# Optimization experiments

Hardware: AMD Instinct MI355X
Metric: run time of the kernel (lower is better)

Reference implementation:

```python
import jax, jax.numpy as jnp
import numpy as np

N_HEADS = 16


def setup_inputs() -> dict:
    key = jax.random.key(0)
    k1, k2 = jax.random.split(key)
    bs, width, length = 8, 3 * N_HEADS * 64, 1024  # C=64 per head
    qkv = jax.random.normal(k1, (bs, width, length), dtype=jnp.float32)
    mask = jax.random.uniform(k2, (bs, length), dtype=jnp.float32)
    return {"qkv": qkv, "mask": mask}


def reference(qkv, mask):
    bs, width, length = qkv.shape
    ch = width // (3 * N_HEADS)
    q, k, v = jnp.split(qkv, 3, axis=1)
    # view(bs*H, ch, T): head index is inner (b*H + h ordering)
    q = q.reshape(bs * N_HEADS, ch, length)
    k = k.reshape(bs * N_HEADS, ch, length)
    v = v.reshape(bs * N_HEADS, ch, length)
    scale = 1.0 / jnp.sqrt(jnp.sqrt(jnp.asarray(ch, dtype=qkv.dtype)))
    # [bs*H, T, T] score matrix
    weight = jnp.einsum('bct,bcs->bts', q * scale, k * scale)
    # torch mask.repeat(n_heads, 1) tiles the batch dim -> jnp.tile
    m = jnp.tile(mask, (N_HEADS, 1))[:, None, :]  # [bs*H, 1, T]
    weight = weight * m
    weight = jax.nn.softmax(weight.astype(jnp.float32), axis=-1).astype(weight.dtype)
    a = jnp.einsum('bts,bcs->bct', weight, v)  # [bs*H, ch, T]
    return a.reshape(bs, N_HEADS * ch, length)
```

## Files before the change

kernel.cpp:

```cpp
#include <hip/hip_runtime.h>
#include <stdint.h>
#include <math.h>

typedef float  f32x4  __attribute__((ext_vector_type(4)));
typedef __bf16 bf16x8 __attribute__((ext_vector_type(8)));
typedef __bf16 bf16x4 __attribute__((ext_vector_type(4)));

#define MFMA16(a, b, c) __builtin_amdgcn_mfma_f32_16x16x32_bf16((a), (b), (c), 0, 0, 0)
#define EXP2(x) __builtin_amdgcn_exp2f(x)

static constexpr int kT = 1024;

static constexpr int kTileEl = 4096;
static constexpr size_t kTensorEl    = (size_t)128 * 16 * kTileEl;
static constexpr size_t kTensorBytes = kTensorEl * 2;

static constexpr int kLS = 72;

__device__ inline void async16(const void* g, void* l) {
  __builtin_amdgcn_global_load_lds(
      (const __attribute__((address_space(1))) void*)g,
      (__attribute__((address_space(3))) void*)l, 16, 0, 0);
}

__global__ __launch_bounds__(256, 4)
void prepass(const float* __restrict__ qkv, const float* __restrict__ mask,
             __bf16* __restrict__ kh, __bf16* __restrict__ vh)
{
  __shared__ float tsK[64 * 65];
  __shared__ float tsV[64 * 65];
  const int tid = threadIdx.x;
  const int bid = blockIdx.x, bh = bid >> 4, tile = bid & 15;
  const int b = bh >> 4, h = bh & 15, t0 = tile * 64;
  const float* __restrict__ kb = qkv + (size_t)(b * 3072 + 1024 + h * 64) * kT;
  const float* __restrict__ vb = qkv + (size_t)(b * 3072 + 2048 + h * 64) * kT;
  const float* __restrict__ mrow = mask + (size_t)(h & 7) * kT;
  const size_t tbase = ((size_t)bh * 16 + tile) * kTileEl;

  const int t4   = (tid & 15) * 4;
  const int crow = tid >> 4;
  const f32x4 m4 = *(const f32x4*)&mrow[t0 + t4];
  #pragma unroll
  for (int i = 0; i < 4; ++i) {
    const int c = i * 16 + crow;
    f32x4 k4 = *(const f32x4*)&kb[(size_t)c * kT + t0 + t4];
    f32x4 v4 = *(const f32x4*)&vb[(size_t)c * kT + t0 + t4];
    k4 *= m4;
    *(f32x4*)&tsK[c * 65 + t4] = k4;
    *(f32x4*)&tsV[c * 65 + t4] = v4;
  }
  __syncthreads();

  #pragma unroll
  for (int i = 0; i < 2; ++i) {
    const int p = i * 256 + tid;
    const int chunk = p >> 6, pl = p & 63;
    const int rr  = (chunk >> 1) * 16 + (pl & 15);
    const int kc0 = (chunk & 1) * 32 + (pl >> 4) * 8;
    bf16x8 k8, v8;
    #pragma unroll
    for (int j = 0; j < 8; ++j) {
      k8[j] = (__bf16)tsK[(kc0 + j) * 65 + rr];
      v8[j] = (__bf16)tsV[rr * 65 + kc0 + j];
    }
    *(bf16x8*)&kh[tbase + (size_t)p * 8] = k8;
    *(bf16x8*)&vh[tbase + (size_t)p * 8] = v8;
  }
}

__global__ __launch_bounds__(256, 3)
void attn_main(const float* __restrict__ qkv,
               const __bf16* __restrict__ kh, const __bf16* __restrict__ vh,
               float* __restrict__ out)
{
  __shared__ __align__(16) char smem[49152];

  const int tid  = threadIdx.x;
  const int lane = tid & 63;
  const int wave = tid >> 6;
  const int quad = lane >> 4;
  const int l15  = lane & 15;

  const int bid = blockIdx.x;
  const int bh  = bid & 127;
  const int tp  = bid >> 7;
  const int b   = bh >> 4;
  const int h   = bh & 15;
  const int t0  = tp * 128;
  const size_t hbase = (size_t)bh * 16;

  {
    const char* g = (const char*)(kh + hbase * kTileEl) + (size_t)lane * 16;
    for (int i = wave; i < 16; i += 4) async16(g + i * 1024, smem + i * 1024);
  }

  bf16x8 qh[2][2], ql[2][2];
  {
    float* ts = (float*)(smem + 32512);
    const float* __restrict__ qb = qkv + (size_t)(b * 3072 + h * 64) * kT;
    const int t4   = (tid & 15) * 4;
    const int crow = tid >> 4;
    const int trow = wave * 16 + l15;
    #pragma unroll
    for (int half = 0; half < 2; ++half) {
      const int tq0 = t0 + half * 64;
      #pragma unroll
      for (int i = 0; i < 4; ++i) {
        const int c = i * 16 + crow;
        f32x4 q4 = *(const f32x4*)&qb[(size_t)c * kT + tq0 + t4];
        q4 *= 0.18033688f;
        *(f32x4*)&ts[c * 65 + t4] = q4;
      }
      __syncthreads();
      #pragma unroll
      for (int kc = 0; kc < 2; ++kc) {
        bf16x8 hf, lf;
        #pragma unroll
        for (int j = 0; j < 8; ++j) {
          float q = ts[(kc * 32 + quad * 8 + j) * 65 + trow];
          __bf16 hi = (__bf16)q;
          hf[j] = hi;
          lf[j] = (__bf16)(q - (float)hi);
        }
        qh[half][kc] = hf;
        ql[half][kc] = lf;
      }
      __syncthreads();
    }
  }

  f32x4 O0[4], O1[4];
  #pragma unroll
  for (int cc = 0; cc < 4; ++cc) {
    O0[cc] = (f32x4){0.f, 0.f, 0.f, 0.f};
    O1[cc] = (f32x4){0.f, 0.f, 0.f, 0.f};
  }
  f32x4 la0 = (f32x4){0.f, 0.f, 0.f, 0.f};
  f32x4 la1 = (f32x4){0.f, 0.f, 0.f, 0.f};

  char* sP0 = smem + 32768 + wave * 4096;
  char* sP1 = sP0 + 2048;
  const int pwr = (l15 << 4) + ((quad & 1) << 3) + ((quad >> 1) << 8);

  for (int p = 0; p < 8; ++p) {
    __syncthreads();

    const __bf16* __restrict__ vt0 = vh + (hbase + 2 * p) * kTileEl;
    const __bf16* __restrict__ vt1 = vt0 + kTileEl;

    bf16x8 vA0[4], vA1[4];
    #pragma unroll
    for (int cc = 0; cc < 4; ++cc)
      vA0[cc] = *(const bf16x8*)&vt0[(size_t)(cc * 2) * 512 + lane * 8];
    #pragma unroll
    for (int cc = 0; cc < 4; ++cc)
      vA1[cc] = *(const bf16x8*)&vt0[(size_t)(cc * 2 + 1) * 512 + lane * 8];

    if (p < 7) {
      const char* g = (const char*)(kh + (hbase + 2 * (p + 1)) * kTileEl) + (size_t)lane * 16;
      char* l = smem + ((p + 1) & 1) * 16384;
      for (int i = wave; i < 16; i += 4) async16(g + i * 1024, l + i * 1024);
    }

    {
      const __bf16* __restrict__ sKt = (const __bf16*)(smem + (p & 1) * 16384);

      #pragma unroll
      for (int sc = 0; sc < 4; ++sc) {
        bf16x8 k0 = *(const bf16x8*)&sKt[(size_t)(sc * 2) * 512 + lane * 8];
        bf16x8 k1 = *(const bf16x8*)&sKt[(size_t)(sc * 2 + 1) * 512 + lane * 8];
        f32x4 a0 = (f32x4){0.f, 0.f, 0.f, 0.f};
        f32x4 a1 = (f32x4){0.f, 0.f, 0.f, 0.f};
        a0 = MFMA16(k0, ql[0][0], a0);
        a1 = MFMA16(k0, ql[1][0], a1);
        a0 = MFMA16(k0, qh[0][0], a0);
        a1 = MFMA16(k0, qh[1][0], a1);
        a0 = MFMA16(k1, ql[0][1], a0);
        a1 = MFMA16(k1, ql[1][1], a1);
        a0 = MFMA16(k1, qh[0][1], a0);
        a1 = MFMA16(k1, qh[1][1], a1);
        f32x4 e0, e1;
        #pragma unroll
        for (int r = 0; r < 4; ++r) {
          e0[r] = EXP2(a0[r]);
          e1[r] = EXP2(a1[r]);
        }
        la0 += e0;
        la1 += e1;
        bf16x4 p0, p1;
        #pragma unroll
        for (int r = 0; r < 4; ++r) {
          p0[r] = (__bf16)e0[r];
          p1[r] = (__bf16)e1[r];
        }
        const int po = ((sc >> 1) << 10) + ((sc & 1) << 9) + pwr;
        *(bf16x4*)(sP0 + po) = p0;
        *(bf16x4*)(sP1 + po) = p1;
      }

      bf16x8 pb00 = *(const bf16x8*)(sP0 + lane * 16);
      bf16x8 pb01 = *(const bf16x8*)(sP0 + 1024 + lane * 16);
      bf16x8 pb10 = *(const bf16x8*)(sP1 + lane * 16);
      bf16x8 pb11 = *(const bf16x8*)(sP1 + 1024 + lane * 16);

      #pragma unroll
      for (int cc = 0; cc < 4; ++cc) {
        O0[cc] = MFMA16(vA0[cc], pb00, O0[cc]);
        O1[cc] = MFMA16(vA0[cc], pb10, O1[cc]);
        O0[cc] = MFMA16(vA1[cc], pb01, O0[cc]);
        O1[cc] = MFMA16(vA1[cc], pb11, O1[cc]);
      }
    }

    {
      const __bf16* __restrict__ sKt = (const __bf16*)(smem + (p & 1) * 16384 + 8192);

      bf16x8 vB0[4], vB1[4];
      #pragma unroll
      for (int cc = 0; cc < 4; ++cc)
        vB0[cc] = *(const bf16x8*)&vt1[(size_t)(cc * 2) * 512 + lane * 8];

      #pragma unroll
      for (int sc = 0; sc < 4; ++sc) {
        bf16x8 k0 = *(const bf16x8*)&sKt[(size_t)(sc * 2) * 512 + lane * 8];
        bf16x8 k1 = *(const bf16x8*)&sKt[(size_t)(sc * 2 + 1) * 512 + lane * 8];
        f32x4 a0 = (f32x4){0.f, 0.f, 0.f, 0.f};
        f32x4 a1 = (f32x4){0.f, 0.f, 0.f, 0.f};
        a0 = MFMA16(k0, ql[0][0], a0);
        a1 = MFMA16(k0, ql[1][0], a1);
        a0 = MFMA16(k0, qh[0][0], a0);
        a1 = MFMA16(k0, qh[1][0], a1);
        a0 = MFMA16(k1, ql[0][1], a0);
        a1 = MFMA16(k1, ql[1][1], a1);
        a0 = MFMA16(k1, qh[0][1], a0);
        a1 = MFMA16(k1, qh[1][1], a1);
        f32x4 e0, e1;
        #pragma unroll
        for (int r = 0; r < 4; ++r) {
          e0[r] = EXP2(a0[r]);
          e1[r] = EXP2(a1[r]);
        }
        la0 += e0;
        la1 += e1;
        bf16x4 p0, p1;
        #pragma unroll
        for (int r = 0; r < 4; ++r) {
          p0[r] = (__bf16)e0[r];
          p1[r] = (__bf16)e1[r];
        }
        const int po = ((sc >> 1) << 10) + ((sc & 1) << 9) + pwr;
        *(bf16x4*)(sP0 + po) = p0;
        *(bf16x4*)(sP1 + po) = p1;
      }

      #pragma unroll
      for (int cc = 0; cc < 4; ++cc)
        vB1[cc] = *(const bf16x8*)&vt1[(size_t)(cc * 2 + 1) * 512 + lane * 8];

      bf16x8 pb00 = *(const bf16x8*)(sP0 + lane * 16);
      bf16x8 pb01 = *(const bf16x8*)(sP0 + 1024 + lane * 16);
      bf16x8 pb10 = *(const bf16x8*)(sP1 + lane * 16);
      bf16x8 pb11 = *(const bf16x8*)(sP1 + 1024 + lane * 16);

      #pragma unroll
      for (int cc = 0; cc < 4; ++cc) {
        O0[cc] = MFMA16(vB0[cc], pb00, O0[cc]);
        O1[cc] = MFMA16(vB0[cc], pb10, O1[cc]);
        O0[cc] = MFMA16(vB1[cc], pb01, O0[cc]);
        O1[cc] = MFMA16(vB1[cc], pb11, O1[cc]);
      }
    }
  }

  float ls0 = la0[0] + la0[1] + la0[2] + la0[3];
  float ls1 = la1[0] + la1[1] + la1[2] + la1[3];
  ls0 += __shfl_xor(ls0, 16);
  ls0 += __shfl_xor(ls0, 32);
  ls1 += __shfl_xor(ls1, 16);
  ls1 += __shfl_xor(ls1, 32);
  const float inv0 = 1.0f / ls0;
  const float inv1 = 1.0f / ls1;

  const int tcol = t0 + wave * 16 + l15;
  float* __restrict__ obase = out + (size_t)b * (1024 * 1024) + (size_t)(h * 64) * kT;
  #pragma unroll
  for (int cc = 0; cc < 4; ++cc) {
    #pragma unroll
    for (int r = 0; r < 4; ++r) {
      const int c = cc * 16 + quad * 4 + r;
      obase[(size_t)c * kT + tcol]      = O0[cc][r] * inv0;
      obase[(size_t)c * kT + tcol + 64] = O1[cc][r] * inv1;
    }
  }
}

__global__ __launch_bounds__(256, 2)
void attn_fused(const float* __restrict__ qkv, const float* __restrict__ mask,
                float* __restrict__ out)
{
  __shared__ __align__(16) __bf16 Ahi[64 * kLS];
  __shared__ __align__(16) __bf16 Alo[64 * kLS];
  __shared__ __align__(16) __bf16 Vhi[64 * kLS];
  __shared__ __align__(16) __bf16 Vlo[64 * kLS];
  __shared__ __align__(16) __bf16 Phi[64 * kLS];
  __shared__ __align__(16) __bf16 Plo[64 * kLS];
  __shared__ __align__(16) float  ms[64];

  const int tid  = threadIdx.x;
  const int lane = tid & 63;
  const int wave = tid >> 6;
  const int quad = lane >> 4;
  const int l15  = lane & 15;

  const int bid = blockIdx.x;
  const int bh  = bid >> 4;
  const int tb  = bid & 15;
  const int b   = bh >> 4;
  const int h   = bh & 15;
  const int t0  = tb * 64;

  const float* __restrict__ qbase = qkv + (size_t)(b * 3072 + h * 64) * kT;
  const float* __restrict__ kbase = qkv + (size_t)(b * 3072 + 1024 + h * 64) * kT;
  const float* __restrict__ vbase = qkv + (size_t)(b * 3072 + 2048 + h * 64) * kT;
  const float* __restrict__ mrow  = mask + (size_t)(h & 7) * kT;

  const int sl = tid & 63;
  const int cg = tid >> 6;

  #pragma unroll
  for (int i = 0; i < 16; ++i) {
    const int c = cg * 16 + i;
    float v  = qbase[(size_t)c * kT + t0 + sl] * 0.125f;
    __bf16 hi = (__bf16)v;
    Ahi[sl * kLS + c] = hi;
    Alo[sl * kLS + c] = (__bf16)(v - (float)hi);
  }
  __syncthreads();

  bf16x8 qh[2], ql[2];
  {
    const int row = (wave * 16 + l15) * kLS;
    #pragma unroll
    for (int kc = 0; kc < 2; ++kc) {
      qh[kc] = *(const bf16x8*)&Ahi[row + kc * 32 + quad * 8];
      ql[kc] = *(const bf16x8*)&Alo[row + kc * 32 + quad * 8];
    }
  }
  __syncthreads();

  f32x4 O[4];
  #pragma unroll
  for (int cc = 0; cc < 4; ++cc) O[cc] = (f32x4){0.f, 0.f, 0.f, 0.f};
  float m_run = -__builtin_inff();
  float l_run = 0.f;

  for (int s0 = 0; s0 < kT; s0 += 64) {
    #pragma unroll
    for (int i = 0; i < 16; ++i) {
      const int c = cg * 16 + i;
      float kv   = kbase[(size_t)c * kT + s0 + sl];
      __bf16 khi = (__bf16)kv;
      Ahi[sl * kLS + c] = khi;
      Alo[sl * kLS + c] = (__bf16)(kv - (float)khi);
      float vv   = vbase[(size_t)c * kT + s0 + sl];
      __bf16 vhi = (__bf16)vv;
      Vhi[c * kLS + sl] = vhi;
      Vlo[c * kLS + sl] = (__bf16)(vv - (float)vhi);
    }
    if (tid < 64) ms[tid] = mrow[s0 + tid];
    __syncthreads();

    f32x4 S[4];
    #pragma unroll
    for (int sc = 0; sc < 4; ++sc) {
      f32x4 acc = (f32x4){0.f, 0.f, 0.f, 0.f};
      #pragma unroll
      for (int kc = 0; kc < 2; ++kc) {
        const int off = (sc * 16 + l15) * kLS + kc * 32 + quad * 8;
        bf16x8 kh8 = *(const bf16x8*)&Ahi[off];
        bf16x8 kl8 = *(const bf16x8*)&Alo[off];
        acc = MFMA16(kh8, ql[kc], acc);
        acc = MFMA16(kl8, qh[kc], acc);
        acc = MFMA16(kh8, qh[kc], acc);
      }
      S[sc] = acc;
    }

    float x[16];
    float tmax = -__builtin_inff();
    #pragma unroll
    for (int sc = 0; sc < 4; ++sc) {
      f32x4 mv = *(const f32x4*)&ms[sc * 16 + quad * 4];
      #pragma unroll
      for (int r = 0; r < 4; ++r) {
        float xv = S[sc][r] * mv[r];
        x[sc * 4 + r] = xv;
        tmax = fmaxf(tmax, xv);
      }
    }
    tmax = fmaxf(tmax, __shfl_xor(tmax, 16));
    tmax = fmaxf(tmax, __shfl_xor(tmax, 32));
    const float mnew  = fmaxf(m_run, tmax);
    const float alpha = __expf(m_run - mnew);
    float tsum = 0.f;
    #pragma unroll
    for (int i = 0; i < 16; ++i) {
      float p = __expf(x[i] - mnew);
      x[i] = p;
      tsum += p;
    }
    tsum += __shfl_xor(tsum, 16);
    tsum += __shfl_xor(tsum, 32);
    l_run = l_run * alpha + tsum;
    m_run = mnew;
    #pragma unroll
    for (int cc = 0; cc < 4; ++cc) O[cc] = O[cc] * alpha;

    const int prow = (wave * 16 + l15) * kLS;
    #pragma unroll
    for (int sc = 0; sc < 4; ++sc) {
      bf16x4 ph, pl;
      #pragma unroll
      for (int r = 0; r < 4; ++r) {
        float p   = x[sc * 4 + r];
        __bf16 hi = (__bf16)p;
        ph[r] = hi;
        pl[r] = (__bf16)(p - (float)hi);
      }
      *(bf16x4*)&Phi[prow + sc * 16 + quad * 4] = ph;
      *(bf16x4*)&Plo[prow + sc * 16 + quad * 4] = pl;
    }
    __syncthreads();

    bf16x8 pbh[2], pbl[2];
    #pragma unroll
    for (int kc = 0; kc < 2; ++kc) {
      pbh[kc] = *(const bf16x8*)&Phi[prow + kc * 32 + quad * 8];
      pbl[kc] = *(const bf16x8*)&Plo[prow + kc * 32 + quad * 8];
    }
    #pragma unroll
    for (int cc = 0; cc < 4; ++cc) {
      #pragma unroll
      for (int kc = 0; kc < 2; ++kc) {
        const int off = (cc * 16 + l15) * kLS + kc * 32 + quad * 8;
        bf16x8 v8 = *(const bf16x8*)&Vhi[off];
        bf16x8 w8 = *(const bf16x8*)&Vlo[off];
        O[cc] = MFMA16(v8, pbl[kc], O[cc]);
        O[cc] = MFMA16(w8, pbh[kc], O[cc]);
        O[cc] = MFMA16(v8, pbh[kc], O[cc]);
      }
    }
    __syncthreads();
  }

  const float inv  = 1.0f / l_run;
  const int   tcol = t0 + wave * 16 + l15;
  float* __restrict__ obase = out + (size_t)b * (1024 * 1024) + (size_t)(h * 64) * kT;
  #pragma unroll
  for (int cc = 0; cc < 4; ++cc) {
    #pragma unroll
    for (int r = 0; r < 4; ++r) {
      const int c = cc * 16 + quad * 4 + r;
      obase[(size_t)c * kT + tcol] = O[cc][r] * inv;
    }
  }
}

extern "C" void kernel_launch(void* const* d_in, const int* in_sizes, int n_in,
                              void* d_out, int out_size, void* d_ws, size_t ws_size,
                              hipStream_t stream)
{
  const float* qkv  = (const float*)d_in[0];
  const float* mask = (const float*)d_in[1];
  float* out = (float*)d_out;
  (void)in_sizes; (void)n_in; (void)out_size;

  if (ws_size >= 2 * kTensorBytes) {
    char* w = (char*)d_ws;
    __bf16* kh = (__bf16*)(w + 0 * kTensorBytes);
    __bf16* vh = (__bf16*)(w + 1 * kTensorBytes);
    prepass<<<dim3(2048), dim3(256), 0, stream>>>(qkv, mask, kh, vh);
    attn_main<<<dim3(1024), dim3(256), 0, stream>>>(qkv, kh, vh, out);
  } else {
    attn_fused<<<dim3(2048), dim3(256), 0, stream>>>(qkv, mask, out);
  }
}
```

Before: 203.9 us.

## Process 256 query rows per block to reuse K/V tiles across four query groups

Each attn_main block now handles 256 query positions instead of 128: it holds four groups of Q fragments and accumulators per wave and launches half as many blocks. Every K tile loaded into LDS and every V fragment read from global memory is reused across four query groups instead of two, which halves K/V traffic per query. In exchange, register pressure and LDS use rise (64KB shared, launch bounds lowered to 2 blocks per CU), and the grid shrinks to 512 blocks. That may underfill the GPU's CUs and lower occupancy.

```diff
diff --git a/kernel.cpp b/kernel.cpp
--- a/kernel.cpp
+++ b/kernel.cpp
@@ -68,12 +68,12 @@
   }
 }
 
-__global__ __launch_bounds__(256, 3)
+__global__ __launch_bounds__(256, 2)
 void attn_main(const float* __restrict__ qkv,
                const __bf16* __restrict__ kh, const __bf16* __restrict__ vh,
                float* __restrict__ out)
 {
-  __shared__ __align__(16) char smem[49152];
+  __shared__ __align__(16) char smem[65536];
 
   const int tid  = threadIdx.x;
   const int lane = tid & 63;
@@ -83,10 +83,10 @@
 
   const int bid = blockIdx.x;
   const int bh  = bid & 127;
-  const int tp  = bid >> 7;
+  const int tq  = bid >> 7;
   const int b   = bh >> 4;
   const int h   = bh & 15;
-  const int t0  = tp * 128;
+  const int t0  = tq * 256;
   const size_t hbase = (size_t)bh * 16;
 
   {
@@ -94,15 +94,15 @@
     for (int i = wave; i < 16; i += 4) async16(g + i * 1024, smem + i * 1024);
   }
 
-  bf16x8 qh[2][2], ql[2][2];
+  bf16x8 qh[4][2], ql[4][2];
   {
-    float* ts = (float*)(smem + 32512);
+    float* ts = (float*)(smem + 32768);
     const float* __restrict__ qb = qkv + (size_t)(b * 3072 + h * 64) * kT;
     const int t4   = (tid & 15) * 4;
     const int crow = tid >> 4;
     const int trow = wave * 16 + l15;
     #pragma unroll
-    for (int half = 0; half < 2; ++half) {
+    for (int half = 0; half < 4; ++half) {
       const int tq0 = t0 + half * 64;
       #pragma unroll
       for (int i = 0; i < 4; ++i) {
@@ -129,17 +129,16 @@
     }
   }
 
-  f32x4 O0[4], O1[4];
-  #pragma unroll
-  for (int cc = 0; cc < 4; ++cc) {
-    O0[cc] = (f32x4){0.f, 0.f, 0.f, 0.f};
-    O1[cc] = (f32x4){0.f, 0.f, 0.f, 0.f};
-  }
-  f32x4 la0 = (f32x4){0.f, 0.f, 0.f, 0.f};
-  f32x4 la1 = (f32x4){0.f, 0.f, 0.f, 0.f};
-
-  char* sP0 = smem + 32768 + wave * 4096;
-  char* sP1 = sP0 + 2048;
+  f32x4 O[4][4];
+  f32x4 la[4];
+  #pragma unroll
+  for (int hh = 0; hh < 4; ++hh) {
+    la[hh] = (f32x4){0.f, 0.f, 0.f, 0.f};
+    #pragma unroll
+    for (int cc = 0; cc < 4; ++cc) O[hh][cc] = (f32x4){0.f, 0.f, 0.f, 0.f};
+  }
+
+  char* sPw = smem + 32768 + wave * 8192;
   const int pwr = (l15 << 4) + ((quad & 1) << 3) + ((quad >> 1) << 8);
 
   for (int p = 0; p < 8; ++p) {
@@ -169,46 +168,40 @@
       for (int sc = 0; sc < 4; ++sc) {
         bf16x8 k0 = *(const bf16x8*)&sKt[(size_t)(sc * 2) * 512 + lane * 8];
         bf16x8 k1 = *(const bf16x8*)&sKt[(size_t)(sc * 2 + 1) * 512 + lane * 8];
-        f32x4 a0 = (f32x4){0.f, 0.f, 0.f, 0.f};
-        f32x4 a1 = (f32x4){0.f, 0.f, 0.f, 0.f};
-        a0 = MFMA16(k0, ql[0][0], a0);
-        a1 = MFMA16(k0, ql[1][0], a1);
-        a0 = MFMA16(k0, qh[0][0], a0);
-        a1 = MFMA16(k0, qh[1][0], a1);
-        a0 = MFMA16(k1, ql[0][1], a0);
-        a1 = MFMA16(k1, ql[1][1], a1);
-        a0 = MFMA16(k1, qh[0][1], a0);
-        a1 = MFMA16(k1, qh[1][1], a1);
-        f32x4 e0, e1;
-        #pragma unroll
-        for (int r = 0; r < 4; ++r) {
-          e0[r] = EXP2(a0[r]);
-          e1[r] = EXP2(a1[r]);
+        f32x4 a[4];
+        #pragma unroll
+        for (int hh = 0; hh < 4; ++hh) a[hh] = (f32x4){0.f, 0.f, 0.f, 0.f};
+        #pragma unroll
+        for (int hh = 0; hh < 4; ++hh) a[hh] = MFMA16(k0, ql[hh][0], a[hh]);
+        #pragma unroll
+        for (int hh = 0; hh < 4; ++hh) a[hh] = MFMA16(k0, qh[hh][0], a[hh]);
+        #pragma unroll
+        for (int hh = 0; hh < 4; ++hh) a[hh] = MFMA16(k1, ql[hh][1], a[hh]);
+        #pragma unroll
+        for (int hh = 0; hh < 4; ++hh) a[hh] = MFMA16(k1, qh[hh][1], a[hh]);
+        const int po = ((sc >> 1) << 10) + ((sc & 1) << 9) + pwr;
+        #pragma unroll
+        for (int hh = 0; hh < 4; ++hh) {
+          f32x4 e;
+          #pragma unroll
+          for (int r = 0; r < 4; ++r) e[r] = EXP2(a[hh][r]);
+          la[hh] += e;
+          bf16x4 pp;
+          #pragma unroll
+          for (int r = 0; r < 4; ++r) pp[r] = (__bf16)e[r];
+          *(bf16x4*)(sPw + hh * 2048 + po) = pp;
         }
-        la0 += e0;
-        la1 += e1;
-        bf16x4 p0, p1;
-        #pragma unroll
-        for (int r = 0; r < 4; ++r) {
-          p0[r] = (__bf16)e0[r];
-          p1[r] = (__bf16)e1[r];
+      }
+
+      #pragma unroll
+      for (int hh = 0; hh < 4; ++hh) {
+        bf16x8 pb0 = *(const bf16x8*)(sPw + hh * 2048 + lane * 16);
+        bf16x8 pb1 = *(const bf16x8*)(sPw + hh * 2048 + 1024 + lane * 16);
+        #pragma unroll
+        for (int cc = 0; cc < 4; ++cc) {
+          O[hh][cc] = MFMA16(vA0[cc], pb0, O[hh][cc]);
+          O[hh][cc] = MFMA16(vA1[cc], pb1, O[hh][cc]);
         }
-        const int po = ((sc >> 1) << 10) + ((sc & 1) << 9) + pwr;
-        *(bf16x4*)(sP0 + po) = p0;
-        *(bf16x4*)(sP1 + po) = p1;
-      }
-
-      bf16x8 pb00 = *(const bf16x8*)(sP0 + lane * 16);
-      bf16x8 pb01 = *(const bf16x8*)(sP0 + 1024 + lane * 16);
-      bf16x8 pb10 = *(const bf16x8*)(sP1 + lane * 16);
-      bf16x8 pb11 = *(const bf16x8*)(sP1 + 1024 + lane * 16);
-
-      #pragma unroll
-      for (int cc = 0; cc < 4; ++cc) {
-        O0[cc] = MFMA16(vA0[cc], pb00, O0[cc]);
-        O1[cc] = MFMA16(vA0[cc], pb10, O1[cc]);
-        O0[cc] = MFMA16(vA1[cc], pb01, O0[cc]);
-        O1[cc] = MFMA16(vA1[cc], pb11, O1[cc]);
       }
     }
 
@@ -224,72 +217,62 @@
       for (int sc = 0; sc < 4; ++sc) {
         bf16x8 k0 = *(const bf16x8*)&sKt[(size_t)(sc * 2) * 512 + lane * 8];
         bf16x8 k1 = *(const bf16x8*)&sKt[(size_t)(sc * 2 + 1) * 512 + lane * 8];
-        f32x4 a0 = (f32x4){0.f, 0.f, 0.f, 0.f};
-        f32x4 a1 = (f32x4){0.f, 0.f, 0.f, 0.f};
-        a0 = MFMA16(k0, ql[0][0], a0);
-        a1 = MFMA16(k0, ql[1][0], a1);
-        a0 = MFMA16(k0, qh[0][0], a0);
-        a1 = MFMA16(k0, qh[1][0], a1);
-        a0 = MFMA16(k1, ql[0][1], a0);
-        a1 = MFMA16(k1, ql[1][1], a1);
-        a0 = MFMA16(k1, qh[0][1], a0);
-        a1 = MFMA16(k1, qh[1][1], a1);
-        f32x4 e0, e1;
-        #pragma unroll
-        for (int r = 0; r < 4; ++r) {
-          e0[r] = EXP2(a0[r]);
-          e1[r] = EXP2(a1[r]);
+        f32x4 a[4];
+        #pragma unroll
+        for (int hh = 0; hh < 4; ++hh) a[hh] = (f32x4){0.f, 0.f, 0.f, 0.f};
+        #pragma unroll
+        for (int hh = 0; hh < 4; ++hh) a[hh] = MFMA16(k0, ql[hh][0], a[hh]);
+        #pragma unroll
+        for (int hh = 0; hh < 4; ++hh) a[hh] = MFMA16(k0, qh[hh][0], a[hh]);
+        #pragma unroll
+        for (int hh = 0; hh < 4; ++hh) a[hh] = MFMA16(k1, ql[hh][1], a[hh]);
+        #pragma unroll
+        for (int hh = 0; hh < 4; ++hh) a[hh] = MFMA16(k1, qh[hh][1], a[hh]);
+        const int po = ((sc >> 1) << 10) + ((sc & 1) << 9) + pwr;
+        #pragma unroll
+        for (int hh = 0; hh < 4; ++hh) {
+          f32x4 e;
+          #pragma unroll
+          for (int r = 0; r < 4; ++r) e[r] = EXP2(a[hh][r]);
+          la[hh] += e;
+          bf16x4 pp;
+          #pragma unroll
+          for (int r = 0; r < 4; ++r) pp[r] = (__bf16)e[r];
+          *(bf16x4*)(sPw + hh * 2048 + po) = pp;
         }
-        la0 += e0;
-        la1 += e1;
-        bf16x4 p0, p1;
-        #pragma unroll
-        for (int r = 0; r < 4; ++r) {
-          p0[r] = (__bf16)e0[r];
-          p1[r] = (__bf16)e1[r];
-        }
-        const int po = ((sc >> 1) << 10) + ((sc & 1) << 9) + pwr;
-        *(bf16x4*)(sP0 + po) = p0;
-        *(bf16x4*)(sP1 + po) = p1;
       }
 
       #pragma unroll
       for (int cc = 0; cc < 4; ++cc)
         vB1[cc] = *(const bf16x8*)&vt1[(size_t)(cc * 2 + 1) * 512 + lane * 8];
 
-      bf16x8 pb00 = *(const bf16x8*)(sP0 + lane * 16);
-      bf16x8 pb01 = *(const bf16x8*)(sP0 + 1024 + lane * 16);
-      bf16x8 pb10 = *(const bf16x8*)(sP1 + lane * 16);
-      bf16x8 pb11 = *(const bf16x8*)(sP1 + 1024 + lane * 16);
-
-      #pragma unroll
-      for (int cc = 0; cc < 4; ++cc) {
-        O0[cc] = MFMA16(vB0[cc], pb00, O0[cc]);
-        O1[cc] = MFMA16(vB0[cc], pb10, O1[cc]);
-        O0[cc] = MFMA16(vB1[cc], pb01, O0[cc]);
-        O1[cc] = MFMA16(vB1[cc], pb11, O1[cc]);
-      }
-    }
-  }
-
-  float ls0 = la0[0] + la0[1] + la0[2] + la0[3];
-  float ls1 = la1[0] + la1[1] + la1[2] + la1[3];
-  ls0 += __shfl_xor(ls0, 16);
-  ls0 += __shfl_xor(ls0, 32);
-  ls1 += __shfl_xor(ls1, 16);
-  ls1 += __shfl_xor(ls1, 32);
-  const float inv0 = 1.0f / ls0;
-  const float inv1 = 1.0f / ls1;
-
-  const int tcol = t0 + wave * 16 + l15;
+      #pragma unroll
+      for (int hh = 0; hh < 4; ++hh) {
+        bf16x8 pb0 = *(const bf16x8*)(sPw + hh * 2048 + lane * 16);
+        bf16x8 pb1 = *(const bf16x8*)(sPw + hh * 2048 + 1024 + lane * 16);
+        #pragma unroll
+        for (int cc = 0; cc < 4; ++cc) {
+          O[hh][cc] = MFMA16(vB0[cc], pb0, O[hh][cc]);
+          O[hh][cc] = MFMA16(vB1[cc], pb1, O[hh][cc]);
+        }
+      }
+    }
+  }
+
   float* __restrict__ obase = out + (size_t)b * (1024 * 1024) + (size_t)(h * 64) * kT;
   #pragma unroll
-  for (int cc = 0; cc < 4; ++cc) {
-    #pragma unroll
-    for (int r = 0; r < 4; ++r) {
-      const int c = cc * 16 + quad * 4 + r;
-      obase[(size_t)c * kT + tcol]      = O0[cc][r] * inv0;
-      obase[(size_t)c * kT + tcol + 64] = O1[cc][r] * inv1;
+  for (int hh = 0; hh < 4; ++hh) {
+    float ls = la[hh][0] + la[hh][1] + la[hh][2] + la[hh][3];
+    ls += __shfl_xor(ls, 16);
+    ls += __shfl_xor(ls, 32);
+    const float inv = 1.0f / ls;
+    const int tcol = t0 + hh * 64 + wave * 16 + l15;
+    #pragma unroll
+    for (int cc = 0; cc < 4; ++cc) {
+      #pragma unroll
+      for (int r = 0; r < 4; ++r) {
+        obase[(size_t)(cc * 16 + quad * 4 + r) * kT + tcol] = O[hh][cc][r] * inv;
+      }
     }
   }
 }
@@ -480,7 +463,7 @@
     __bf16* kh = (__bf16*)(w + 0 * kTensorBytes);
     __bf16* vh = (__bf16*)(w + 1 * kTensorBytes);
     prepass<<<dim3(2048), dim3(256), 0, stream>>>(qkv, mask, kh, vh);
-    attn_main<<<dim3(1024), dim3(256), 0, stream>>>(qkv, kh, vh, out);
+    attn_main<<<dim3(512), dim3(256), 0, stream>>>(qkv, kh, vh, out);
   } else {
     attn_fused<<<dim3(2048), dim3(256), 0, stream>>>(qkv, mask, out);
   }
```

Result: no change. 203.3 us (-0.3%).
